# Kernel optimization log

Measured on AMD Instinct MI355X. Metric: run time of the kernel, lower is better.

The kernel has to match this reference:

```python
import jax, jax.numpy as jnp
import numpy as np

VOCAB = 50257
C = 8  # n_dim_categories
B, T = 4, 4096


def setup_inputs() -> dict:
    key = jax.random.key(0)
    k1, k2, k3 = jax.random.split(key, 3)
    token_ids = jax.random.randint(k1, (B, T), 0, VOCAB)
    dim_embedding = jax.random.normal(k2, (VOCAB, C), dtype=jnp.float32)
    compatibility = jax.random.normal(k3, (C, C), dtype=jnp.float32) * 0.1
    return {"token_ids": token_ids, "dim_embedding": dim_embedding,
            "compatibility": compatibility}


def reference(token_ids, dim_embedding, compatibility):
    # (B,T,C): embedding lookup then softmax over categories
    dim_probs = jax.nn.softmax(dim_embedding[token_ids], axis=-1)
    # bilinear compatibility over all T x T token pairs -> (B,T,T)
    compat = jnp.einsum('btc,cd,bsd->bts', dim_probs, compatibility, dim_probs)
    mask_bias = jax.nn.sigmoid(compat) * 2 - 1
    return mask_bias
```

## Files before the change

kernel.cpp:

```cpp
#include <hip/hip_runtime.h>
#include <hip/hip_bf16.h>

typedef float f32x4 __attribute__((ext_vector_type(4)));

namespace {
constexpr int kB = 4;
constexpr int kT = 4096;
constexpr int kC = 8;
constexpr int kN = kB * kT;
constexpr int kTRows = 16;
constexpr int kSPerThread = 4;
constexpr int kBlockThreads = 256;
constexpr int kSTile = kBlockThreads * kSPerThread;
}

__global__ __launch_bounds__(256) void dam_prep(const int* __restrict__ token_ids,
                                                const float* __restrict__ emb,
                                                const float* __restrict__ cmat,
                                                float* __restrict__ p_ws,
                                                float* __restrict__ z_ws) {
    int tid = blockIdx.x * blockDim.x + threadIdx.x;
    if (tid >= kN) return;
    int tok = token_ids[tid];
    const f32x4* row = reinterpret_cast<const f32x4*>(emb) + (size_t)tok * 2;
    f32x4 e0 = row[0], e1 = row[1];
    float e[kC] = {e0.x, e0.y, e0.z, e0.w, e1.x, e1.y, e1.z, e1.w};
    float m = e[0];
#pragma unroll
    for (int i = 1; i < kC; ++i) m = fmaxf(m, e[i]);
    float p[kC], sum = 0.f;
#pragma unroll
    for (int i = 0; i < kC; ++i) { p[i] = __expf(e[i] - m); sum += p[i]; }
    float inv = 1.0f / sum;
#pragma unroll
    for (int i = 0; i < kC; ++i) p[i] *= inv;
    float z[kC];
#pragma unroll
    for (int c = 0; c < kC; ++c) {
        float acc = 0.f;
#pragma unroll
        for (int d = 0; d < kC; ++d) acc = fmaf(cmat[c * kC + d], p[d], acc);
        z[c] = -acc;
    }
    f32x4* po = reinterpret_cast<f32x4*>(p_ws) + (size_t)tid * 2;
    po[0] = f32x4{p[0], p[1], p[2], p[3]};
    po[1] = f32x4{p[4], p[5], p[6], p[7]};
    f32x4* zo = reinterpret_cast<f32x4*>(z_ws) + (size_t)tid * 2;
    zo[0] = f32x4{z[0], z[1], z[2], z[3]};
    zo[1] = f32x4{z[4], z[5], z[6], z[7]};
}

__global__ __launch_bounds__(256) void dam_mask(const float* __restrict__ p_ws,
                                                const float* __restrict__ z_ws,
                                                float* __restrict__ out) {
    const int b = blockIdx.z;
    const int t0 = blockIdx.y * kTRows;
    const int s0 = blockIdx.x * kSTile;
    __shared__ f32x4 p_lds[kTRows * 2];
    const int tid = threadIdx.x;
    if (tid < kTRows * 2)
        p_lds[tid] = reinterpret_cast<const f32x4*>(p_ws + ((size_t)(b * kT + t0)) * kC)[tid];
    __syncthreads();

    const int s = s0 + tid * kSPerThread;
    const f32x4* zr = reinterpret_cast<const f32x4*>(z_ws) + ((size_t)(b * kT) + s) * 2;
    float z[kSPerThread][kC];
#pragma unroll
    for (int j = 0; j < kSPerThread; ++j) {
        f32x4 a = zr[j * 2 + 0];
        f32x4 c = zr[j * 2 + 1];
        z[j][0] = a.x; z[j][1] = a.y; z[j][2] = a.z; z[j][3] = a.w;
        z[j][4] = c.x; z[j][5] = c.y; z[j][6] = c.z; z[j][7] = c.w;
    }

    float* orow = out + ((size_t)(b * kT + t0)) * kT + s;
#pragma unroll
    for (int tt = 0; tt < kTRows; ++tt) {
        f32x4 p0 = p_lds[tt * 2 + 0];
        f32x4 p1 = p_lds[tt * 2 + 1];
        float pr[kC] = {p0.x, p0.y, p0.z, p0.w, p1.x, p1.y, p1.z, p1.w};
        float r[kSPerThread];
#pragma unroll
        for (int j = 0; j < kSPerThread; ++j) {
            float acc = 0.f;
#pragma unroll
            for (int i = 0; i < kC; ++i) acc = fmaf(pr[i], z[j][i], acc);
            float ex = __expf(acc);
            r[j] = (1.f - ex) * __builtin_amdgcn_rcpf(1.f + ex);
        }
        f32x4 ov = {r[0], r[1], r[2], r[3]};
        *reinterpret_cast<f32x4*>(orow + (size_t)tt * kT) = ov;
    }
}

extern "C" void kernel_launch(void* const* d_in, const int* in_sizes, int n_in,
                              void* d_out, int out_size, void* d_ws, size_t ws_size,
                              hipStream_t stream) {
    const int* token_ids = (const int*)d_in[0];
    const float* emb     = (const float*)d_in[1];
    const float* cmat    = (const float*)d_in[2];
    float* out  = (float*)d_out;
    float* p_ws = (float*)d_ws;
    float* z_ws = p_ws + (size_t)kN * kC;

    dam_prep<<<(kN + 255) / 256, 256, 0, stream>>>(token_ids, emb, cmat, p_ws, z_ws);
    dim3 grid(kT / kSTile, kT / kTRows, kB);
    dam_mask<<<grid, kBlockThreads, 0, stream>>>(p_ws, z_ws, out);
}
```

Measured before the change: 53.39 us.

## Fuse softmax and compatibility projection into mask kernel, drop prep launch

Removes the separate prep kernel and its workspace round trip. Each mask block now gathers embedding rows for its 16 t-rows and 1024 s-columns, computes the softmax and the C-projection in place, then writes the output tile. This saves a kernel launch and workspace traffic, but repeats the softmax and 8x8 matvec for every s-column in every t-block, which is 256 times redundant per batch, and does random embedding gathers in each block. The softmax division is also replaced with a hardware reciprocal.

```diff
diff --git a/kernel.cpp b/kernel.cpp
--- a/kernel.cpp
+++ b/kernel.cpp
@@ -7,71 +7,71 @@
 constexpr int kB = 4;
 constexpr int kT = 4096;
 constexpr int kC = 8;
-constexpr int kN = kB * kT;
 constexpr int kTRows = 16;
 constexpr int kSPerThread = 4;
 constexpr int kBlockThreads = 256;
 constexpr int kSTile = kBlockThreads * kSPerThread;
 }
 
-__global__ __launch_bounds__(256) void dam_prep(const int* __restrict__ token_ids,
-                                                const float* __restrict__ emb,
-                                                const float* __restrict__ cmat,
-                                                float* __restrict__ p_ws,
-                                                float* __restrict__ z_ws) {
-    int tid = blockIdx.x * blockDim.x + threadIdx.x;
-    if (tid >= kN) return;
-    int tok = token_ids[tid];
-    const f32x4* row = reinterpret_cast<const f32x4*>(emb) + (size_t)tok * 2;
-    f32x4 e0 = row[0], e1 = row[1];
-    float e[kC] = {e0.x, e0.y, e0.z, e0.w, e1.x, e1.y, e1.z, e1.w};
+__device__ __forceinline__ void softmax8(const float e[kC], float p[kC]) {
     float m = e[0];
 #pragma unroll
     for (int i = 1; i < kC; ++i) m = fmaxf(m, e[i]);
-    float p[kC], sum = 0.f;
+    float sum = 0.f;
 #pragma unroll
     for (int i = 0; i < kC; ++i) { p[i] = __expf(e[i] - m); sum += p[i]; }
-    float inv = 1.0f / sum;
+    float inv = __builtin_amdgcn_rcpf(sum);
 #pragma unroll
     for (int i = 0; i < kC; ++i) p[i] *= inv;
-    float z[kC];
-#pragma unroll
-    for (int c = 0; c < kC; ++c) {
-        float acc = 0.f;
-#pragma unroll
-        for (int d = 0; d < kC; ++d) acc = fmaf(cmat[c * kC + d], p[d], acc);
-        z[c] = -acc;
-    }
-    f32x4* po = reinterpret_cast<f32x4*>(p_ws) + (size_t)tid * 2;
-    po[0] = f32x4{p[0], p[1], p[2], p[3]};
-    po[1] = f32x4{p[4], p[5], p[6], p[7]};
-    f32x4* zo = reinterpret_cast<f32x4*>(z_ws) + (size_t)tid * 2;
-    zo[0] = f32x4{z[0], z[1], z[2], z[3]};
-    zo[1] = f32x4{z[4], z[5], z[6], z[7]};
 }
 
-__global__ __launch_bounds__(256) void dam_mask(const float* __restrict__ p_ws,
-                                                const float* __restrict__ z_ws,
-                                                float* __restrict__ out) {
+__device__ __forceinline__ void load_emb_row(const float* __restrict__ emb, int tok,
+                                             float e[kC]) {
+    const f32x4* row = reinterpret_cast<const f32x4*>(emb) + (size_t)tok * 2;
+    f32x4 e0 = row[0], e1 = row[1];
+    e[0] = e0.x; e[1] = e0.y; e[2] = e0.z; e[3] = e0.w;
+    e[4] = e1.x; e[5] = e1.y; e[6] = e1.z; e[7] = e1.w;
+}
+
+__global__ __launch_bounds__(256) void dam_fused(const int* __restrict__ token_ids,
+                                                 const float* __restrict__ emb,
+                                                 const float* __restrict__ cmat,
+                                                 float* __restrict__ out) {
     const int b = blockIdx.z;
     const int t0 = blockIdx.y * kTRows;
     const int s0 = blockIdx.x * kSTile;
+    const int tid = threadIdx.x;
+
     __shared__ f32x4 p_lds[kTRows * 2];
-    const int tid = threadIdx.x;
-    if (tid < kTRows * 2)
-        p_lds[tid] = reinterpret_cast<const f32x4*>(p_ws + ((size_t)(b * kT + t0)) * kC)[tid];
-    __syncthreads();
+
+    if (tid < kTRows) {
+        int tok = token_ids[b * kT + t0 + tid];
+        float e[kC], p[kC];
+        load_emb_row(emb, tok, e);
+        softmax8(e, p);
+        p_lds[tid * 2 + 0] = f32x4{p[0], p[1], p[2], p[3]};
+        p_lds[tid * 2 + 1] = f32x4{p[4], p[5], p[6], p[7]};
+    }
 
     const int s = s0 + tid * kSPerThread;
-    const f32x4* zr = reinterpret_cast<const f32x4*>(z_ws) + ((size_t)(b * kT) + s) * 2;
+    int4 toks = *reinterpret_cast<const int4*>(&token_ids[b * kT + s]);
+    int tokj[kSPerThread] = {toks.x, toks.y, toks.z, toks.w};
     float z[kSPerThread][kC];
 #pragma unroll
     for (int j = 0; j < kSPerThread; ++j) {
-        f32x4 a = zr[j * 2 + 0];
-        f32x4 c = zr[j * 2 + 1];
-        z[j][0] = a.x; z[j][1] = a.y; z[j][2] = a.z; z[j][3] = a.w;
-        z[j][4] = c.x; z[j][5] = c.y; z[j][6] = c.z; z[j][7] = c.w;
+        float e[kC], q[kC];
+        load_emb_row(emb, tokj[j], e);
+        softmax8(e, q);
+#pragma unroll
+        for (int c = 0; c < kC; ++c) {
+            float acc = 0.f;
+#pragma unroll
+            for (int d = 0; d < kC; ++d) acc = fmaf(cmat[c * kC + d], q[d], acc);
+            z[j][c] = -acc;
+        }
     }
+
+    __syncthreads();
 
     float* orow = out + ((size_t)(b * kT + t0)) * kT + s;
 #pragma unroll
@@ -99,11 +99,8 @@
     const int* token_ids = (const int*)d_in[0];
     const float* emb     = (const float*)d_in[1];
     const float* cmat    = (const float*)d_in[2];
-    float* out  = (float*)d_out;
-    float* p_ws = (float*)d_ws;
-    float* z_ws = p_ws + (size_t)kN * kC;
+    float* out = (float*)d_out;
 
-    dam_prep<<<(kN + 255) / 256, 256, 0, stream>>>(token_ids, emb, cmat, p_ws, z_ws);
     dim3 grid(kT / kSTile, kT / kTRows, kB);
-    dam_mask<<<grid, kBlockThreads, 0, stream>>>(p_ws, z_ws, out);
+    dam_fused<<<grid, kBlockThreads, 0, stream>>>(token_ids, emb, cmat, out);
 }
```

After: 56.30 us. 5.5% more time.
